# Performance work log

Hardware: AMD Instinct MI355X
Metric: run time of the kernel (lower is better)

Reference implementation:

```python
import jax, jax.numpy as jnp
import numpy as np

L, B, D_IN = 2048, 32, 1024
DENSE, HID = 256, 128
NUM_CLASSES = 2
NT = NUM_CLASSES + 2  # + START, STOP tags
START, STOP = NT - 2, NT - 1
IMPOSSIBLE = -1e4


def setup_inputs() -> dict:
    key = jax.random.key(0)
    ks = jax.random.split(key, 14)
    s = 0.05
    src = jax.random.uniform(ks[0], (L, B, D_IN), dtype=jnp.float32)
    fc1_w = jax.random.normal(ks[1], (DENSE, D_IN), jnp.float32) * s
    fc1_b = jax.random.normal(ks[2], (DENSE,), jnp.float32) * s
    w_ih_f = jax.random.normal(ks[3], (4 * HID, DENSE), jnp.float32) * s
    w_hh_f = jax.random.normal(ks[4], (4 * HID, HID), jnp.float32) * s
    b_ih_f = jax.random.normal(ks[5], (4 * HID,), jnp.float32) * s
    b_hh_f = jax.random.normal(ks[6], (4 * HID,), jnp.float32) * s
    w_ih_b = jax.random.normal(ks[7], (4 * HID, DENSE), jnp.float32) * s
    w_hh_b = jax.random.normal(ks[8], (4 * HID, HID), jnp.float32) * s
    b_ih_b = jax.random.normal(ks[9], (4 * HID,), jnp.float32) * s
    b_hh_b = jax.random.normal(ks[10], (4 * HID,), jnp.float32) * s
    crf_w = jax.random.normal(ks[11], (NT, 2 * HID), jnp.float32) * s
    crf_b = jax.random.normal(ks[12], (NT,), jnp.float32) * s
    transitions = jax.random.normal(ks[13], (NT, NT), jnp.float32)
    transitions = transitions.at[START, :].set(IMPOSSIBLE)  # no transition TO start
    transitions = transitions.at[:, STOP].set(IMPOSSIBLE)   # no transition FROM stop
    return dict(src=src, fc1_w=fc1_w, fc1_b=fc1_b,
                w_ih_f=w_ih_f, w_hh_f=w_hh_f, b_ih_f=b_ih_f, b_hh_f=b_hh_f,
                w_ih_b=w_ih_b, w_hh_b=w_hh_b, b_ih_b=b_ih_b, b_hh_b=b_hh_b,
                crf_w=crf_w, crf_b=crf_b, transitions=transitions)


def _lstm_dir(x, w_ih, w_hh, b_ih, b_hh):
    # x: [L, B, D]; PyTorch gate order i, f, g, o
    pre = jnp.einsum('lbd,hd->lbh', x, w_ih) + b_ih + b_hh  # [L, B, 4H]
    h_dim = w_hh.shape[1]
    bsz = x.shape[1]

    def step(carry, p):
        h, c = carry
        g = p + h @ w_hh.T
        i, f, gg, o = jnp.split(g, 4, axis=-1)
        c = jax.nn.sigmoid(f) * c + jax.nn.sigmoid(i) * jnp.tanh(gg)
        h = jax.nn.sigmoid(o) * jnp.tanh(c)
        return (h, c), h

    init = (jnp.zeros((bsz, h_dim), x.dtype), jnp.zeros((bsz, h_dim), x.dtype))
    _, hs = jax.lax.scan(step, init, pre)
    return hs  # [L, B, H]


def reference(src, fc1_w, fc1_b, w_ih_f, w_hh_f, b_ih_f, b_hh_f,
              w_ih_b, w_hh_b, b_ih_b, b_hh_b, crf_w, crf_b, transitions):
    masks = (jnp.sum(src, axis=2) > 0).T.astype(src.dtype)  # [B, L]
    x = jax.nn.relu(jnp.einsum('lbd,od->lbo', src, fc1_w) + fc1_b)  # [L,B,DENSE]
    hf = _lstm_dir(x, w_ih_f, w_hh_f, b_ih_f, b_hh_f)
    hb = _lstm_dir(x[::-1], w_ih_b, w_hh_b, b_ih_b, b_hh_b)[::-1]
    feats = jnp.concatenate([hf, hb], axis=-1)  # [L, B, 2H] (dropout = eval identity)
    emit = jnp.einsum('lbh,ch->lbc', feats, crf_w) + crf_b  # [L, B, NT]

    bsz = src.shape[1]
    init_score = jnp.full((bsz, NT), IMPOSSIBLE, emit.dtype).at[:, START].set(0.0)

    def vstep(max_score, inp):
        e_t, m_t = inp  # [B, NT], [B]
        acc = max_score[:, None, :] + transitions[None]  # [B, to, from]
        bp = jnp.argmax(acc, axis=-1)                    # [B, NT]
        new = jnp.max(acc, axis=-1) + e_t
        m = m_t[:, None]
        return new * m + max_score * (1.0 - m), bp

    final, bps = jax.lax.scan(vstep, init_score, (emit, masks.T))  # bps: [L, B, NT]
    final = final + transitions[STOP]
    best_score = jnp.max(final, axis=-1)   # [B]
    best_tag = jnp.argmax(final, axis=-1)  # [B]

    def bstep(tag, bp_t):
        prev = jnp.take_along_axis(bp_t, tag[:, None], axis=1)[:, 0]
        return prev, prev

    _, prevs = jax.lax.scan(bstep, best_tag, bps[1:], reverse=True)  # tags t=0..L-2
    tags = jnp.concatenate([prevs, best_tag[None]], axis=0).T  # [B, L]
    return best_score, tags
```

## Files before the change

kernel.cpp:

```cpp
#include <hip/hip_runtime.h>
#include <hip/hip_bf16.h>
#include <stdint.h>

#define L_SEQ 2048
#define BATCH 32
#define D_IN 1024
#define DENSE 256
#define HID 128
#define GATES 512
#define NT 4
#define START_TAG 2
#define STOP_TAG 3
#define IMPOSSIBLE -10000.0f

template<bool RELU, bool DUAL>
__global__ __launch_bounds__(256)
void gemm_nt(const float* __restrict__ A, const float* __restrict__ Bw,
             const float* __restrict__ b1, const float* __restrict__ b2,
             float* __restrict__ C, int M, int N, int K)
{
    __shared__ __align__(16) float As[16][132];
    __shared__ __align__(16) float Bs[16][132];

    const int tid = threadIdx.x;
    const int tx = tid & 15;
    const int ty = tid >> 4;
    const int m0 = blockIdx.x * 128;
    const int n0 = blockIdx.y * 128;

    const int lrow = tid >> 2;
    const int lcol = (tid & 3) * 4;

    float acc[8][8];
#pragma unroll
    for (int i = 0; i < 8; ++i)
#pragma unroll
        for (int j = 0; j < 8; ++j) acc[i][j] = 0.f;

    for (int k0 = 0; k0 < K; k0 += 16) {
#pragma unroll
        for (int p = 0; p < 2; ++p) {
            const int row = lrow + p * 64;
            float4 av = *(const float4*)&A[(size_t)(m0 + row) * K + k0 + lcol];
            As[lcol + 0][row] = av.x; As[lcol + 1][row] = av.y;
            As[lcol + 2][row] = av.z; As[lcol + 3][row] = av.w;
            float4 bv = *(const float4*)&Bw[(size_t)(n0 + row) * K + k0 + lcol];
            Bs[lcol + 0][row] = bv.x; Bs[lcol + 1][row] = bv.y;
            Bs[lcol + 2][row] = bv.z; Bs[lcol + 3][row] = bv.w;
        }
        __syncthreads();
#pragma unroll
        for (int kk = 0; kk < 16; ++kk) {
            float a[8], b[8];
            *(float4*)&a[0] = *(const float4*)&As[kk][ty * 8];
            *(float4*)&a[4] = *(const float4*)&As[kk][ty * 8 + 4];
            *(float4*)&b[0] = *(const float4*)&Bs[kk][tx * 8];
            *(float4*)&b[4] = *(const float4*)&Bs[kk][tx * 8 + 4];
#pragma unroll
            for (int i = 0; i < 8; ++i)
#pragma unroll
                for (int j = 0; j < 8; ++j)
                    acc[i][j] = fmaf(a[i], b[j], acc[i][j]);
        }
        __syncthreads();
    }

    float bia[8];
#pragma unroll
    for (int j = 0; j < 8; ++j) {
        int col = n0 + tx * 8 + j;
        bia[j] = b1[col] + (DUAL ? b2[col] : 0.f);
    }
#pragma unroll
    for (int r = 0; r < 8; ++r) {
        int row = m0 + ty * 8 + r;
        float v[8];
#pragma unroll
        for (int j = 0; j < 8; ++j) {
            v[j] = acc[r][j] + bia[j];
            if (RELU) v[j] = fmaxf(v[j], 0.f);
        }
        float* cp = &C[(size_t)row * N + n0 + tx * 8];
        *(float4*)&cp[0] = make_float4(v[0], v[1], v[2], v[3]);
        *(float4*)&cp[4] = make_float4(v[4], v[5], v[6], v[7]);
    }
}

__device__ __forceinline__ float sigf(float x) { return 1.f / (1.f + expf(-x)); }

__global__ __launch_bounds__(512)
void lstm_kernel(const float* __restrict__ preF, const float* __restrict__ preB,
                 const float* __restrict__ wF, const float* __restrict__ wB,
                 float* __restrict__ hF, float* __restrict__ hB)
{
    const int g = blockIdx.x;
    const int dir = g >> 5;
    const int b = g & 31;
    const float* pre = dir ? preB : preF;
    const float* W   = dir ? wB : wF;
    float* hout      = dir ? hB : hF;

    const int t = threadIdx.x;

    float w[128];
#pragma unroll
    for (int k = 0; k < 128; k += 4)
        *(float4*)&w[k] = *(const float4*)&W[(size_t)t * 128 + k];

    __shared__ __align__(16) float h_s[128];
    __shared__ __align__(16) float c_s[128];
    __shared__ __align__(16) float g_s[512];

    if (t < 128) { h_s[t] = 0.f; c_s[t] = 0.f; }
    __syncthreads();

    int tt0 = dir ? (L_SEQ - 1) : 0;
    float pre_next = pre[((size_t)tt0 * BATCH + b) * GATES + t];

    for (int step = 0; step < L_SEQ; ++step) {
        const int tt = dir ? (L_SEQ - 1 - step) : step;
        float pre_cur = pre_next;
        if (step + 1 < L_SEQ) {
            int tn = dir ? (L_SEQ - 2 - step) : (step + 1);
            pre_next = pre[((size_t)tn * BATCH + b) * GATES + t];
        }

        float acc = pre_cur;
#pragma unroll
        for (int k = 0; k < 128; k += 4) {
            float4 hv = *(const float4*)&h_s[k];
            acc = fmaf(w[k + 0], hv.x, acc);
            acc = fmaf(w[k + 1], hv.y, acc);
            acc = fmaf(w[k + 2], hv.z, acc);
            acc = fmaf(w[k + 3], hv.w, acc);
        }
        g_s[t] = acc;
        __syncthreads();

        if (t < 128) {
            float iv = g_s[t];
            float fv = g_s[128 + t];
            float gv = g_s[256 + t];
            float ov = g_s[384 + t];
            float c  = sigf(fv) * c_s[t] + sigf(iv) * tanhf(gv);
            float h  = sigf(ov) * tanhf(c);
            c_s[t] = c;
            h_s[t] = h;
            hout[((size_t)tt * BATCH + b) * HID + t] = h;
        }
        __syncthreads();
    }
}

__global__ __launch_bounds__(256)
void emit_kernel(const float* __restrict__ hf, const float* __restrict__ hb,
                 const float* __restrict__ crf_w, const float* __restrict__ crf_b,
                 float* __restrict__ emit)
{
    const int idx = blockIdx.x * 256 + threadIdx.x;
    const int r = idx >> 2;
    const int c = idx & 3;
    const float* wf = &crf_w[c * 256];
    float acc = crf_b[c];
#pragma unroll 4
    for (int k = 0; k < 128; k += 4) {
        float4 hv = *(const float4*)&hf[(size_t)r * 128 + k];
        float4 wv = *(const float4*)&wf[k];
        acc = fmaf(hv.x, wv.x, acc); acc = fmaf(hv.y, wv.y, acc);
        acc = fmaf(hv.z, wv.z, acc); acc = fmaf(hv.w, wv.w, acc);
    }
#pragma unroll 4
    for (int k = 0; k < 128; k += 4) {
        float4 hv = *(const float4*)&hb[(size_t)r * 128 + k];
        float4 wv = *(const float4*)&wf[128 + k];
        acc = fmaf(hv.x, wv.x, acc); acc = fmaf(hv.y, wv.y, acc);
        acc = fmaf(hv.z, wv.z, acc); acc = fmaf(hv.w, wv.w, acc);
    }
    emit[idx] = acc;
}

__global__ __launch_bounds__(64)
void viterbi_kernel(const float* __restrict__ emit, const float* __restrict__ trans,
                    float* __restrict__ out)
{
    const int lane = threadIdx.x;
    const int b_loc = lane >> 2;
    const int i = lane & 3;
    const int b = blockIdx.x * 16 + b_loc;
    const int base = lane & ~3;

    __shared__ uint8_t bp_s[L_SEQ * 16];
    __shared__ uint8_t tag_s[L_SEQ * 16];

    float T0 = trans[i * 4 + 0];
    float T1 = trans[i * 4 + 1];
    float T2 = trans[i * 4 + 2];
    float T3 = trans[i * 4 + 3];
    float tstop = trans[STOP_TAG * 4 + i];

    float s = (i == START_TAG) ? 0.f : IMPOSSIBLE;

    float e_cur = emit[(size_t)0 * BATCH * NT + b * NT + i];
    for (int t = 0; t < L_SEQ; ++t) {
        float e_next = 0.f;
        if (t + 1 < L_SEQ)
            e_next = emit[(size_t)(t + 1) * BATCH * NT + b * NT + i];

        float s0 = __shfl(s, base + 0, 64);
        float s1 = __shfl(s, base + 1, 64);
        float s2 = __shfl(s, base + 2, 64);
        float s3 = __shfl(s, base + 3, 64);

        float a0 = s0 + T0, a1 = s1 + T1, a2 = s2 + T2, a3 = s3 + T3;
        float best = a0; int arg = 0;
        if (a1 > best) { best = a1; arg = 1; }
        if (a2 > best) { best = a2; arg = 2; }
        if (a3 > best) { best = a3; arg = 3; }

        s = best + e_cur;
        e_cur = e_next;

        int A0 = __shfl(arg, base + 0, 64);
        int A1 = __shfl(arg, base + 1, 64);
        int A2 = __shfl(arg, base + 2, 64);
        int A3 = __shfl(arg, base + 3, 64);
        if (i == 0)
            bp_s[t * 16 + b_loc] = (uint8_t)(A0 | (A1 << 2) | (A2 << 4) | (A3 << 6));
    }

    float f = s + tstop;
    float f0 = __shfl(f, base + 0, 64);
    float f1 = __shfl(f, base + 1, 64);
    float f2 = __shfl(f, base + 2, 64);
    float f3 = __shfl(f, base + 3, 64);
    float best = f0; int btag = 0;
    if (f1 > best) { best = f1; btag = 1; }
    if (f2 > best) { best = f2; btag = 2; }
    if (f3 > best) { best = f3; btag = 3; }

    if (i == 0) {
        out[b] = best;
        int tag = btag;
        tag_s[(L_SEQ - 1) * 16 + b_loc] = (uint8_t)tag;
        for (int t = L_SEQ - 1; t >= 1; --t) {
            uint8_t byte = bp_s[t * 16 + b_loc];
            tag = (byte >> (2 * tag)) & 3;
            tag_s[(t - 1) * 16 + b_loc] = (uint8_t)tag;
        }
    }
    __syncthreads();

    float* tout = out + BATCH;
    for (int bb = 0; bb < 16; ++bb) {
        int bg = blockIdx.x * 16 + bb;
        for (int t0 = lane; t0 < L_SEQ; t0 += 64)
            tout[(size_t)bg * L_SEQ + t0] = (float)tag_s[t0 * 16 + bb];
    }
}

extern "C" void kernel_launch(void* const* d_in, const int* in_sizes, int n_in,
                              void* d_out, int out_size, void* d_ws, size_t ws_size,
                              hipStream_t stream)
{
    const float* src    = (const float*)d_in[0];
    const float* fc1_w  = (const float*)d_in[1];
    const float* fc1_b  = (const float*)d_in[2];
    const float* w_ih_f = (const float*)d_in[3];
    const float* w_hh_f = (const float*)d_in[4];
    const float* b_ih_f = (const float*)d_in[5];
    const float* b_hh_f = (const float*)d_in[6];
    const float* w_ih_b = (const float*)d_in[7];
    const float* w_hh_b = (const float*)d_in[8];
    const float* b_ih_b = (const float*)d_in[9];
    const float* b_hh_b = (const float*)d_in[10];
    const float* crf_w  = (const float*)d_in[11];
    const float* crf_b  = (const float*)d_in[12];
    const float* trans  = (const float*)d_in[13];

    char* ws = (char*)d_ws;
    const size_t MB = 1024 * 1024;
    float* x    = (float*)(ws);
    float* preF = (float*)(ws + 64 * MB);
    float* preB = (float*)(ws + 192 * MB);
    float* hf   = (float*)(ws);
    float* hb   = (float*)(ws + 32 * MB);
    float* emit = (float*)(ws + 64 * MB);

    const int M = L_SEQ * BATCH;

    {
        dim3 grid(M / 128, DENSE / 128);
        gemm_nt<true, false><<<grid, 256, 0, stream>>>(src, fc1_w, fc1_b, nullptr,
                                                       x, M, DENSE, D_IN);
    }
    {
        dim3 grid(M / 128, GATES / 128);
        gemm_nt<false, true><<<grid, 256, 0, stream>>>(x, w_ih_f, b_ih_f, b_hh_f,
                                                       preF, M, GATES, DENSE);
        gemm_nt<false, true><<<grid, 256, 0, stream>>>(x, w_ih_b, b_ih_b, b_hh_b,
                                                       preB, M, GATES, DENSE);
    }
    lstm_kernel<<<64, 512, 0, stream>>>(preF, preB, w_hh_f, w_hh_b, hf, hb);

    emit_kernel<<<(M * NT) / 256, 256, 0, stream>>>(hf, hb, crf_w, crf_b, emit);

    viterbi_kernel<<<2, 64, 0, stream>>>(emit, trans, (float*)d_out);
}
```

Baseline: 4.060 ms.

## Double-buffer GEMM tiles and streamline LSTM recurrence step

The GEMM now uses two shared-memory buffers and prefetches the next K-slice into registers while computing on the current one, so each iteration needs one barrier instead of two. The LSTM kernel keeps the cell state in a register, splits the 128-term dot product into four independent accumulators, walks the pre-activation pointer incrementally, and replaces __syncthreads with a raw s_waitcnt plus s_barrier. It also moves the global h store after the second barrier and adds a two-blocks-per-CU launch bound. The aim is to shorten the sequential per-step latency of the recurrence, which dominates runtime. The inline asm barriers depend on the hardware memory ordering for correctness, and the launch bound may constrain registers for the 128-float weight array.

```diff
diff --git a/kernel.cpp b/kernel.cpp
--- a/kernel.cpp
+++ b/kernel.cpp
@@ -19,8 +19,8 @@
              const float* __restrict__ b1, const float* __restrict__ b2,
              float* __restrict__ C, int M, int N, int K)
 {
-    __shared__ __align__(16) float As[16][132];
-    __shared__ __align__(16) float Bs[16][132];
+    __shared__ __align__(16) float As[2][16][132];
+    __shared__ __align__(16) float Bs[2][16][132];
 
     const int tid = threadIdx.x;
     const int tx = tid & 15;
@@ -31,38 +31,66 @@
     const int lrow = tid >> 2;
     const int lcol = (tid & 3) * 4;
 
+    const float* aptr = &A[(size_t)(m0 + lrow) * K + lcol];
+    const float* bptr = &Bw[(size_t)(n0 + lrow) * K + lcol];
+    const size_t rstride = (size_t)64 * K;
+
     float acc[8][8];
 #pragma unroll
     for (int i = 0; i < 8; ++i)
 #pragma unroll
         for (int j = 0; j < 8; ++j) acc[i][j] = 0.f;
 
+    {
+        float4 a0 = *(const float4*)(aptr);
+        float4 a1 = *(const float4*)(aptr + rstride);
+        float4 v0 = *(const float4*)(bptr);
+        float4 v1 = *(const float4*)(bptr + rstride);
+        As[0][lcol + 0][lrow] = a0.x; As[0][lcol + 1][lrow] = a0.y;
+        As[0][lcol + 2][lrow] = a0.z; As[0][lcol + 3][lrow] = a0.w;
+        As[0][lcol + 0][lrow + 64] = a1.x; As[0][lcol + 1][lrow + 64] = a1.y;
+        As[0][lcol + 2][lrow + 64] = a1.z; As[0][lcol + 3][lrow + 64] = a1.w;
+        Bs[0][lcol + 0][lrow] = v0.x; Bs[0][lcol + 1][lrow] = v0.y;
+        Bs[0][lcol + 2][lrow] = v0.z; Bs[0][lcol + 3][lrow] = v0.w;
+        Bs[0][lcol + 0][lrow + 64] = v1.x; Bs[0][lcol + 1][lrow + 64] = v1.y;
+        Bs[0][lcol + 2][lrow + 64] = v1.z; Bs[0][lcol + 3][lrow + 64] = v1.w;
+    }
+    __syncthreads();
+
+    int buf = 0;
     for (int k0 = 0; k0 < K; k0 += 16) {
-#pragma unroll
-        for (int p = 0; p < 2; ++p) {
-            const int row = lrow + p * 64;
-            float4 av = *(const float4*)&A[(size_t)(m0 + row) * K + k0 + lcol];
-            As[lcol + 0][row] = av.x; As[lcol + 1][row] = av.y;
-            As[lcol + 2][row] = av.z; As[lcol + 3][row] = av.w;
-            float4 bv = *(const float4*)&Bw[(size_t)(n0 + row) * K + k0 + lcol];
-            Bs[lcol + 0][row] = bv.x; Bs[lcol + 1][row] = bv.y;
-            Bs[lcol + 2][row] = bv.z; Bs[lcol + 3][row] = bv.w;
-        }
-        __syncthreads();
+        const int kn = (k0 + 16 < K) ? (k0 + 16) : k0;
+        float4 na0 = *(const float4*)(aptr + kn);
+        float4 na1 = *(const float4*)(aptr + kn + rstride);
+        float4 nb0 = *(const float4*)(bptr + kn);
+        float4 nb1 = *(const float4*)(bptr + kn + rstride);
+
 #pragma unroll
         for (int kk = 0; kk < 16; ++kk) {
             float a[8], b[8];
-            *(float4*)&a[0] = *(const float4*)&As[kk][ty * 8];
-            *(float4*)&a[4] = *(const float4*)&As[kk][ty * 8 + 4];
-            *(float4*)&b[0] = *(const float4*)&Bs[kk][tx * 8];
-            *(float4*)&b[4] = *(const float4*)&Bs[kk][tx * 8 + 4];
+            *(float4*)&a[0] = *(const float4*)&As[buf][kk][ty * 8];
+            *(float4*)&a[4] = *(const float4*)&As[buf][kk][ty * 8 + 4];
+            *(float4*)&b[0] = *(const float4*)&Bs[buf][kk][tx * 8];
+            *(float4*)&b[4] = *(const float4*)&Bs[buf][kk][tx * 8 + 4];
 #pragma unroll
             for (int i = 0; i < 8; ++i)
 #pragma unroll
                 for (int j = 0; j < 8; ++j)
                     acc[i][j] = fmaf(a[i], b[j], acc[i][j]);
         }
+
+        const int nb = buf ^ 1;
+        As[nb][lcol + 0][lrow] = na0.x; As[nb][lcol + 1][lrow] = na0.y;
+        As[nb][lcol + 2][lrow] = na0.z; As[nb][lcol + 3][lrow] = na0.w;
+        As[nb][lcol + 0][lrow + 64] = na1.x; As[nb][lcol + 1][lrow + 64] = na1.y;
+        As[nb][lcol + 2][lrow + 64] = na1.z; As[nb][lcol + 3][lrow + 64] = na1.w;
+        Bs[nb][lcol + 0][lrow] = nb0.x; Bs[nb][lcol + 1][lrow] = nb0.y;
+        Bs[nb][lcol + 2][lrow] = nb0.z; Bs[nb][lcol + 3][lrow] = nb0.w;
+        Bs[nb][lcol + 0][lrow + 64] = nb1.x; Bs[nb][lcol + 1][lrow + 64] = nb1.y;
+        Bs[nb][lcol + 2][lrow + 64] = nb1.z; Bs[nb][lcol + 3][lrow + 64] = nb1.w;
+
         __syncthreads();
+        buf = nb;
     }
 
     float bia[8];
@@ -88,7 +116,7 @@
 
 __device__ __forceinline__ float sigf(float x) { return 1.f / (1.f + expf(-x)); }
 
-__global__ __launch_bounds__(512)
+__global__ __launch_bounds__(512, 2)
 void lstm_kernel(const float* __restrict__ preF, const float* __restrict__ preB,
                  const float* __restrict__ wF, const float* __restrict__ wB,
                  float* __restrict__ hF, float* __restrict__ hB)
@@ -108,47 +136,51 @@
         *(float4*)&w[k] = *(const float4*)&W[(size_t)t * 128 + k];
 
     __shared__ __align__(16) float h_s[128];
-    __shared__ __align__(16) float c_s[128];
     __shared__ __align__(16) float g_s[512];
 
-    if (t < 128) { h_s[t] = 0.f; c_s[t] = 0.f; }
+    float c_reg = 0.f;
+    if (t < 128) h_s[t] = 0.f;
     __syncthreads();
 
-    int tt0 = dir ? (L_SEQ - 1) : 0;
-    float pre_next = pre[((size_t)tt0 * BATCH + b) * GATES + t];
+    const float* prow = pre + ((size_t)(dir ? (L_SEQ - 1) : 0) * BATCH + b) * GATES + t;
+    const intptr_t pstep = (dir ? -(intptr_t)1 : (intptr_t)1) * (intptr_t)(BATCH * GATES);
+
+    float pre_next = *prow;
 
     for (int step = 0; step < L_SEQ; ++step) {
         const int tt = dir ? (L_SEQ - 1 - step) : step;
         float pre_cur = pre_next;
-        if (step + 1 < L_SEQ) {
-            int tn = dir ? (L_SEQ - 2 - step) : (step + 1);
-            pre_next = pre[((size_t)tn * BATCH + b) * GATES + t];
-        }
-
-        float acc = pre_cur;
+        if (step + 1 < L_SEQ) prow += pstep;
+        pre_next = *prow;
+
+        float a0 = pre_cur, a1 = 0.f, a2 = 0.f, a3 = 0.f;
 #pragma unroll
         for (int k = 0; k < 128; k += 4) {
             float4 hv = *(const float4*)&h_s[k];
-            acc = fmaf(w[k + 0], hv.x, acc);
-            acc = fmaf(w[k + 1], hv.y, acc);
-            acc = fmaf(w[k + 2], hv.z, acc);
-            acc = fmaf(w[k + 3], hv.w, acc);
-        }
-        g_s[t] = acc;
-        __syncthreads();
-
+            a0 = fmaf(w[k + 0], hv.x, a0);
+            a1 = fmaf(w[k + 1], hv.y, a1);
+            a2 = fmaf(w[k + 2], hv.z, a2);
+            a3 = fmaf(w[k + 3], hv.w, a3);
+        }
+        g_s[t] = (a0 + a1) + (a2 + a3);
+
+        asm volatile("s_waitcnt lgkmcnt(0)\n\ts_barrier" ::: "memory");
+
+        float h_keep = 0.f;
         if (t < 128) {
             float iv = g_s[t];
-            float fv = g_s[128 + t];
-            float gv = g_s[256 + t];
-            float ov = g_s[384 + t];
-            float c  = sigf(fv) * c_s[t] + sigf(iv) * tanhf(gv);
-            float h  = sigf(ov) * tanhf(c);
-            c_s[t] = c;
-            h_s[t] = h;
-            hout[((size_t)tt * BATCH + b) * HID + t] = h;
-        }
-        __syncthreads();
+            float fv = g_s[t + 128];
+            float gv = g_s[t + 256];
+            float ov = g_s[t + 384];
+            c_reg = sigf(fv) * c_reg + sigf(iv) * tanhf(gv);
+            h_keep = sigf(ov) * tanhf(c_reg);
+            h_s[t] = h_keep;
+        }
+
+        asm volatile("s_waitcnt lgkmcnt(0)\n\ts_barrier" ::: "memory");
+
+        if (t < 128)
+            hout[((size_t)tt * BATCH + b) * HID + t] = h_keep;
     }
 }
 
```

Measured after the change: 4.782 ms. 17.8% more time.
